# Performance work log

Hardware: AMD Instinct MI355X
Metric: run time of the kernel (lower is better)

Reference implementation:

```python
import jax, jax.numpy as jnp
import numpy as np

NEG_BIG = -9e15

def setup_inputs() -> dict:
    key = jax.random.key(0)
    kx, ka, kW, k1, k2 = jax.random.split(key, 5)
    B, N, F, H, D = 8, 1024, 1024, 16, 64
    x = jax.random.normal(kx, (B, N, F), dtype=jnp.float32)
    adj = jax.random.randint(ka, (B, N, N), 0, 2, dtype=jnp.int32)
    # xavier_uniform with gain=1.414
    gain = 1.414
    limW = gain * np.sqrt(6.0 / (F + D))
    lima = gain * np.sqrt(6.0 / (D + 1))
    W = jax.random.uniform(kW, (H, F, D), minval=-limW, maxval=limW, dtype=jnp.float32)
    a1 = jax.random.uniform(k1, (H, D), minval=-lima, maxval=lima, dtype=jnp.float32)
    a2 = jax.random.uniform(k2, (H, D), minval=-lima, maxval=lima, dtype=jnp.float32)
    return {"x": x, "adj": adj, "W": W, "a1": a1, "a2": a2}

def reference(x, adj, W, a1, a2):
    alpha = 0.2
    # Wh: [B, H, N, D]
    Wh = jnp.einsum('bnf,hfd->bhnd', x, W)
    f1 = jnp.einsum('bhnd,hd->bhn', Wh, a1)  # [B,H,N]
    f2 = jnp.einsum('bhnd,hd->bhn', Wh, a2)  # [B,H,N]
    e = f1[:, :, :, None] + f2[:, :, None, :]          # [B,H,N,N]
    e = jnp.where(e > 0, e, alpha * e)                  # leaky relu
    mask = (adj > 0)[:, None, :, :]                     # [B,1,N,N]
    scores = jnp.where(mask, e, NEG_BIG)
    attn = jax.nn.softmax(scores, axis=-1)              # [B,H,N,N]
    # dropout omitted (inference / training=False)
    h_prime = jnp.einsum('bhnm,bhmd->bhnd', attn, Wh)   # [B,H,N,D]
    B, H, N, D = h_prime.shape
    # concat heads along feature dim (matches torch.cat over dim=2)
    y = jnp.transpose(h_prime, (0, 2, 1, 3)).reshape(B, N, H * D)
    return y
```

## Files before the change

kernel.cpp:

```cpp
#include <hip/hip_runtime.h>

typedef float    f32x4 __attribute__((ext_vector_type(4)));
typedef short    s16x8 __attribute__((ext_vector_type(8)));
typedef _Float16 f16x8 __attribute__((ext_vector_type(8)));
typedef _Float16 f16x4 __attribute__((ext_vector_type(4)));
typedef unsigned int   u32x4 __attribute__((ext_vector_type(4)));


__device__ __forceinline__ unsigned short bf16rne(float f){
  unsigned u = __float_as_uint(f);
  return (unsigned short)((u + 0x7FFFu + ((u >> 16) & 1u)) >> 16);
}

__global__ __launch_bounds__(256) void prep_kernel(const int* __restrict__ adj,
    const float* __restrict__ x, const float* __restrict__ W,
    unsigned* __restrict__ maskb, unsigned short* __restrict__ xb,
    unsigned short* __restrict__ Wt)
{
  const int bid = blockIdx.x, tid = threadIdx.x;
  if (bid < 1024) {
    const int lane = tid & 63;
    int gw = (bid * 256 + tid) >> 6;
    for (int s = gw; s < 131072; s += 4096) {
      int a = adj[(size_t)s * 64 + lane];
      unsigned long long m = __ballot(a > 0);
      if (lane == 0) {
        maskb[s * 2]     = (unsigned)m;
        maskb[s * 2 + 1] = (unsigned)(m >> 32);
      }
    }
  } else if (bid < 5120) {
    int idx = ((bid - 1024) * 256 + tid) * 8;
    f32x4 v0 = *reinterpret_cast<const f32x4*>(&x[idx]);
    f32x4 v1 = *reinterpret_cast<const f32x4*>(&x[idx + 4]);
    u32x4 o;
    o[0] = (unsigned)bf16rne(v0[0]) | ((unsigned)bf16rne(v0[1]) << 16);
    o[1] = (unsigned)bf16rne(v0[2]) | ((unsigned)bf16rne(v0[3]) << 16);
    o[2] = (unsigned)bf16rne(v1[0]) | ((unsigned)bf16rne(v1[1]) << 16);
    o[3] = (unsigned)bf16rne(v1[2]) | ((unsigned)bf16rne(v1[3]) << 16);
    *reinterpret_cast<u32x4*>(&xb[idx]) = o;
  } else {
    __shared__ float t[16][17];
    int rel = bid - 5120;
    int f0 = (rel & 63) * 16, d0 = ((rel >> 6) & 3) * 16, hh = rel >> 8;
    const int tx = tid & 15, ty = tid >> 4;
    t[ty][tx] = W[(size_t)hh * 65536 + (size_t)(f0 + ty) * 64 + (d0 + tx)];
    __syncthreads();
    float v = t[tx][ty];
    size_t o = (size_t)(hh * 64 + d0 + ty) * 1024 + (f0 + tx);
    Wt[o] = bf16rne(v);
  }
}

#define GSTAGE(BUF, K0) { \
  _Pragma("unroll") \
  for (int r = 0; r < 2; ++r) { \
    int flat = r * 256 + tid; int row = flat >> 2; int o8 = (flat & 3) << 3; \
    *reinterpret_cast<u32x4*>(&Ah[BUF][row * 40 + o8]) = \
        *reinterpret_cast<const u32x4*>(&xb[(size_t)(m0 + row) * 1024 + (K0) + o8]); \
  } \
  _Pragma("unroll") \
  for (int r = 0; r < 2; ++r) { \
    int flat = r * 256 + tid; int row = flat >> 2; int o8 = (flat & 3) << 3; \
    *reinterpret_cast<u32x4*>(&Bh[BUF][row * 40 + o8]) = \
        *reinterpret_cast<const u32x4*>(&Btg[(size_t)(n0 + row) * 1024 + (K0) + o8]); \
  } }

__global__ __launch_bounds__(256, 3) void gemm_kernel(const unsigned short* __restrict__ xb,
    const unsigned short* __restrict__ Btg,
    const float* __restrict__ a1, const float* __restrict__ a2,
    _Float16* __restrict__ WhT, float* __restrict__ f1, float* __restrict__ f2)
{
  __shared__ unsigned short Ah[2][128 * 40], Bh[2][128 * 40];
  const int tid  = threadIdx.x;
  const int lane = tid & 63, wave = tid >> 6;
  const int m0 = blockIdx.x * 128, n0 = blockIdx.y * 128;
  const int wm = (wave & 1) * 64, wn = (wave >> 1) * 64;
  const int rA = lane & 15, kg = lane >> 4;

  f32x4 acc[4][4] = {};

  GSTAGE(0, 0);
  __syncthreads();
  int cur = 0;
  for (int k0 = 0; k0 < 1024; k0 += 32) {
    if (k0 + 32 < 1024) { GSTAGE(cur ^ 1, k0 + 32); }

    s16x8 ah[4], bh[4];
#pragma unroll
    for (int i = 0; i < 4; ++i)
      ah[i] = *reinterpret_cast<const s16x8*>(&Ah[cur][(wm + i * 16 + rA) * 40 + kg * 8]);
#pragma unroll
    for (int j = 0; j < 4; ++j)
      bh[j] = *reinterpret_cast<const s16x8*>(&Bh[cur][(wn + j * 16 + rA) * 40 + kg * 8]);
#pragma unroll
    for (int i = 0; i < 4; ++i)
#pragma unroll
      for (int j = 0; j < 4; ++j)
        acc[i][j] = __builtin_amdgcn_mfma_f32_16x16x32_bf16(ah[i], bh[j], acc[i][j], 0, 0, 0);
    __syncthreads();
    cur ^= 1;
  }

#pragma unroll
  for (int i = 0; i < 4; ++i) {
    int gm0 = m0 + wm + i * 16 + kg * 4;
#pragma unroll
    for (int j = 0; j < 4; ++j) {
      int gn = n0 + wn + j * 16 + rA;
      int bb = gm0 >> 10, nn = gm0 & 1023;
      int hh = gn >> 6,  dd = gn & 63;
      f16x4 hv;
#pragma unroll
      for (int jj = 0; jj < 4; ++jj) hv[jj] = (_Float16)acc[i][j][jj];
      *reinterpret_cast<f16x4*>(&WhT[((size_t)((bb * 16 + hh) * 64 + dd) << 10) + nn]) = hv;
    }
  }

  const int hw = (n0 + wn) >> 6;
  float a1v[4], a2v[4];
#pragma unroll
  for (int j = 0; j < 4; ++j) {
    int d = j * 16 + rA;
    a1v[j] = a1[hw * 64 + d];
    a2v[j] = a2[hw * 64 + d];
  }
#pragma unroll
  for (int i = 0; i < 4; ++i) {
#pragma unroll
    for (int jj = 0; jj < 4; ++jj) {
      float s1 = 0.f, s2 = 0.f;
#pragma unroll
      for (int j = 0; j < 4; ++j) {
        float v = acc[i][j][jj];
        s1 += v * a1v[j];
        s2 += v * a2v[j];
      }
#pragma unroll
      for (int off = 1; off < 16; off <<= 1) {
        s1 += __shfl_xor(s1, off);
        s2 += __shfl_xor(s2, off);
      }
      if (rA == 0) {
        int gm = m0 + wm + i * 16 + kg * 4 + jj;
        int bb = gm >> 10, nn = gm & 1023;
        size_t o = (size_t)(bb * 16 + hw) * 1024 + nn;
        f1[o] = s1;
        f2[o] = s2;
      }
    }
  }
}

#define PSTAGE(BUF, M0) { \
  _Pragma("unroll") \
  for (int r = 0; r < 2; ++r) { \
    int flat = r * 256 + tid; int d = flat >> 3; int o = (flat & 7) << 3; \
    *reinterpret_cast<u32x4*>(&Bsh[BUF][d * 72 + o]) = \
        *reinterpret_cast<const u32x4*>(&whtb[(size_t)d * 1024 + (M0) + o]); \
  } }

__global__ __launch_bounds__(256, 4) void pv_kernel(const _Float16* __restrict__ WhT,
    const float* __restrict__ f1, const float* __restrict__ f2,
    const unsigned* __restrict__ maskb, float* __restrict__ y)
{
  const int tid = threadIdx.x, lane = tid & 63, wave = tid >> 6;
  const int rb = blockIdx.x, h = blockIdx.y, b = blockIdx.z;
  const int bh = b * 16 + h;
  const int n0 = rb * 128;
  const _Float16* whtb = WhT + ((size_t)bh << 16);

  __shared__ _Float16 Bsh[2][64 * 72];
  __shared__ float Cs[1024], Ds[1024];
  __shared__ float smx[4];
  __shared__ unsigned long long lutm[16];

  const float K = 1.44269504f;

  float pmax;
  {
    f32x4 fv = *reinterpret_cast<const f32x4*>(&f2[(size_t)bh * 1024 + tid * 4]);
    f32x4 sv, cv, dv;
#pragma unroll
    for (int e = 0; e < 4; ++e) {
      sv[e] = fv[e] * K;
      cv[e] = __builtin_amdgcn_exp2f(sv[e]);
      dv[e] = __builtin_amdgcn_exp2f(0.2f * sv[e]);
    }
    *reinterpret_cast<f32x4*>(&Cs[tid * 4]) = cv;
    *reinterpret_cast<f32x4*>(&Ds[tid * 4]) = dv;
    pmax = fmaxf(fmaxf(sv[0], sv[1]), fmaxf(sv[2], sv[3]));
  }
#pragma unroll
  for (int off = 32; off; off >>= 1) pmax = fmaxf(pmax, __shfl_xor(pmax, off));
  if (lane == 0) smx[wave] = pmax;
  if (tid < 16) {
    unsigned lo = ((tid & 1) ? 0xFFFFu : 0u) | ((tid & 2) ? 0xFFFF0000u : 0u);
    unsigned hi = ((tid & 4) ? 0xFFFFu : 0u) | ((tid & 8) ? 0xFFFF0000u : 0u);
    lutm[tid] = ((unsigned long long)hi << 32) | lo;
  }
  __syncthreads();

  const float m2s = fmaxf(fmaxf(smx[0], smx[1]), fmaxf(smx[2], smx[3]));

  const int rA = lane & 15, kg = lane >> 4;
  const int wrow = wave * 32;
  f32x4 acc[2][4] = {};
  f32x4 dacc[2] = {};
  int   rloc[2];
  float At[2], Bt[2];
  const unsigned* mrow[2];
#pragma unroll
  for (int t = 0; t < 2; ++t) {
    rloc[t] = wrow + t * 16 + rA;
    float f1p = f1[(size_t)bh * 1024 + n0 + rloc[t]] * K;
    float sf = f1p + m2s;
    float Mp = fmaxf(sf, 0.2f * sf);
    At[t] = __builtin_amdgcn_exp2f(f1p - Mp);
    Bt[t] = __builtin_amdgcn_exp2f(0.2f * f1p - Mp);
    mrow[t] = maskb + ((size_t)(b << 10) + n0 + rloc[t]) * 32;
  }
  f16x8 ones;
#pragma unroll
  for (int e = 0; e < 8; ++e) ones[e] = (_Float16)1.0f;

  uint2 mwcur[2], mwnext[2];
#pragma unroll
  for (int t = 0; t < 2; ++t)
    mwcur[t] = *reinterpret_cast<const uint2*>(&mrow[t][0]);
  PSTAGE(0, 0);
  __syncthreads();
  int cur = 0;

  for (int m0 = 0; m0 < 1024; m0 += 64) {
    if (m0 + 64 < 1024) {
      PSTAGE(cur ^ 1, m0 + 64);
#pragma unroll
      for (int t = 0; t < 2; ++t)
        mwnext[t] = *reinterpret_cast<const uint2*>(&mrow[t][(m0 + 64) >> 5]);
    }
#pragma unroll
    for (int ks = 0; ks < 2; ++ks) {
      const int kc = m0 + ks * 32 + kg * 8;
      f32x4 ca = *reinterpret_cast<const f32x4*>(&Cs[kc]);
      f32x4 cb = *reinterpret_cast<const f32x4*>(&Cs[kc + 4]);
      f32x4 da = *reinterpret_cast<const f32x4*>(&Ds[kc]);
      f32x4 db = *reinterpret_cast<const f32x4*>(&Ds[kc + 4]);
      f16x8 pa[2];
#pragma unroll
      for (int t = 0; t < 2; ++t) {
        unsigned mw = (&mwcur[t].x)[ks] >> (kg * 8);
        f16x8 pt;
#pragma unroll
        for (int jj = 0; jj < 8; ++jj) {
          float C = (jj < 4) ? ca[jj] : cb[jj - 4];
          float D = (jj < 4) ? da[jj] : db[jj - 4];
          pt[jj] = (_Float16)fmaxf(At[t] * C, Bt[t] * D);
        }
        u32x4 pw = __builtin_bit_cast(u32x4, pt);
        unsigned long long mq0 = lutm[mw & 15u];
        unsigned long long mq1 = lutm[(mw >> 4) & 15u];
        pw[0] &= (unsigned)mq0;  pw[1] &= (unsigned)(mq0 >> 32);
        pw[2] &= (unsigned)mq1;  pw[3] &= (unsigned)(mq1 >> 32);
        pa[t] = __builtin_bit_cast(f16x8, pw);
        dacc[t] = __builtin_amdgcn_mfma_f32_16x16x32_f16(pa[t], ones, dacc[t], 0, 0, 0);
      }
#pragma unroll
      for (int j = 0; j < 4; ++j) {
        f16x8 bf = *reinterpret_cast<const f16x8*>(&Bsh[cur][(j * 16 + rA) * 72 + ks * 32 + kg * 8]);
        acc[0][j] = __builtin_amdgcn_mfma_f32_16x16x32_f16(pa[0], bf, acc[0][j], 0, 0, 0);
        acc[1][j] = __builtin_amdgcn_mfma_f32_16x16x32_f16(pa[1], bf, acc[1][j], 0, 0, 0);
      }
    }
    __syncthreads();
    cur ^= 1;
#pragma unroll
    for (int t = 0; t < 2; ++t) mwcur[t] = mwnext[t];
  }

#pragma unroll
  for (int t = 0; t < 2; ++t) {
    f32x4 rd;
#pragma unroll
    for (int jj = 0; jj < 4; ++jj) rd[jj] = dacc[t][jj] > 0.f ? 1.0f / dacc[t][jj] : 0.f;
#pragma unroll
    for (int j = 0; j < 4; ++j) {
#pragma unroll
      for (int jj = 0; jj < 4; ++jj) {
        int row = wrow + t * 16 + kg * 4 + jj;
        int n = n0 + row, d = j * 16 + rA;
        y[(((size_t)b * 1024 + n) << 10) + h * 64 + d] = acc[t][j][jj] * rd[jj];
      }
    }
  }
}

extern "C" void kernel_launch(void* const* d_in, const int* in_sizes, int n_in,
                              void* d_out, int out_size, void* d_ws, size_t ws_size,
                              hipStream_t stream)
{
  const float* x  = (const float*)d_in[0];
  const int*   adj = (const int*)d_in[1];
  const float* W  = (const float*)d_in[2];
  const float* a1 = (const float*)d_in[3];
  const float* a2 = (const float*)d_in[4];
  float* y = (float*)d_out;

  char* ws = (char*)d_ws;
  unsigned short* Wt = (unsigned short*)(ws);
  unsigned*       maskb = (unsigned*)(ws + ((size_t)2 << 20));
  float* f1   = (float*)(ws + ((size_t)3 << 20));
  float* f2   = (float*)(ws + ((size_t)3 << 20) + ((size_t)512 << 10));
  _Float16* WhT = (_Float16*)(ws + ((size_t)4 << 20));
  unsigned short* xb = (unsigned short*)(ws + ((size_t)20 << 20));

  prep_kernel<<<9216, 256, 0, stream>>>(adj, x, W, maskb, xb, Wt);
  gemm_kernel<<<dim3(64, 8), 256, 0, stream>>>(xb, Wt, a1, a2, WhT, f1, f2);
  pv_kernel<<<dim3(8, 16, 8), 256, 0, stream>>>(WhT, f1, f2, maskb, y);
}
```

Baseline: 93.23 us.

## Halve GEMM N-tile to 64, raise occupancy, and use packed f16 conversion in PV

The projection GEMM tile shrinks from 128x128 to 128x64 with four waves each owning 32 rows. This doubles the grid and cuts per-thread accumulators so the kernel can raise its launch bound to four blocks per CU. The aim is more resident waves and more blocks to fill the CUs, at the cost of more reloads of the A tile. In the PV kernel the C/D loads are hoisted ahead of both k-steps, and the f16 conversion now uses packed round-toward-zero cvt_pkrtz. That conversion cuts instruction count but changes rounding from round-to-nearest.

```diff
diff --git a/kernel.cpp b/kernel.cpp
--- a/kernel.cpp
+++ b/kernel.cpp
@@ -4,6 +4,7 @@
 typedef short    s16x8 __attribute__((ext_vector_type(8)));
 typedef _Float16 f16x8 __attribute__((ext_vector_type(8)));
 typedef _Float16 f16x4 __attribute__((ext_vector_type(4)));
+typedef _Float16 f16x2 __attribute__((ext_vector_type(2)));
 typedef unsigned int   u32x4 __attribute__((ext_vector_type(4)));
 
 
@@ -59,26 +60,24 @@
     *reinterpret_cast<u32x4*>(&Ah[BUF][row * 40 + o8]) = \
         *reinterpret_cast<const u32x4*>(&xb[(size_t)(m0 + row) * 1024 + (K0) + o8]); \
   } \
-  _Pragma("unroll") \
-  for (int r = 0; r < 2; ++r) { \
-    int flat = r * 256 + tid; int row = flat >> 2; int o8 = (flat & 3) << 3; \
+  { int row = tid >> 2; int o8 = (tid & 3) << 3; \
     *reinterpret_cast<u32x4*>(&Bh[BUF][row * 40 + o8]) = \
         *reinterpret_cast<const u32x4*>(&Btg[(size_t)(n0 + row) * 1024 + (K0) + o8]); \
   } }
 
-__global__ __launch_bounds__(256, 3) void gemm_kernel(const unsigned short* __restrict__ xb,
+__global__ __launch_bounds__(256, 4) void gemm_kernel(const unsigned short* __restrict__ xb,
     const unsigned short* __restrict__ Btg,
     const float* __restrict__ a1, const float* __restrict__ a2,
     _Float16* __restrict__ WhT, float* __restrict__ f1, float* __restrict__ f2)
 {
-  __shared__ unsigned short Ah[2][128 * 40], Bh[2][128 * 40];
+  __shared__ unsigned short Ah[2][128 * 40], Bh[2][64 * 40];
   const int tid  = threadIdx.x;
   const int lane = tid & 63, wave = tid >> 6;
-  const int m0 = blockIdx.x * 128, n0 = blockIdx.y * 128;
-  const int wm = (wave & 1) * 64, wn = (wave >> 1) * 64;
+  const int m0 = blockIdx.x * 128, n0 = blockIdx.y * 64;
+  const int wm = wave * 32;
   const int rA = lane & 15, kg = lane >> 4;
 
-  f32x4 acc[4][4] = {};
+  f32x4 acc[2][4] = {};
 
   GSTAGE(0, 0);
   __syncthreads();
@@ -86,15 +85,15 @@
   for (int k0 = 0; k0 < 1024; k0 += 32) {
     if (k0 + 32 < 1024) { GSTAGE(cur ^ 1, k0 + 32); }
 
-    s16x8 ah[4], bh[4];
-#pragma unroll
-    for (int i = 0; i < 4; ++i)
+    s16x8 ah[2], bh[4];
+#pragma unroll
+    for (int i = 0; i < 2; ++i)
       ah[i] = *reinterpret_cast<const s16x8*>(&Ah[cur][(wm + i * 16 + rA) * 40 + kg * 8]);
 #pragma unroll
     for (int j = 0; j < 4; ++j)
-      bh[j] = *reinterpret_cast<const s16x8*>(&Bh[cur][(wn + j * 16 + rA) * 40 + kg * 8]);
-#pragma unroll
-    for (int i = 0; i < 4; ++i)
+      bh[j] = *reinterpret_cast<const s16x8*>(&Bh[cur][(j * 16 + rA) * 40 + kg * 8]);
+#pragma unroll
+    for (int i = 0; i < 2; ++i)
 #pragma unroll
       for (int j = 0; j < 4; ++j)
         acc[i][j] = __builtin_amdgcn_mfma_f32_16x16x32_bf16(ah[i], bh[j], acc[i][j], 0, 0, 0);
@@ -103,11 +102,11 @@
   }
 
 #pragma unroll
-  for (int i = 0; i < 4; ++i) {
+  for (int i = 0; i < 2; ++i) {
     int gm0 = m0 + wm + i * 16 + kg * 4;
 #pragma unroll
     for (int j = 0; j < 4; ++j) {
-      int gn = n0 + wn + j * 16 + rA;
+      int gn = n0 + j * 16 + rA;
       int bb = gm0 >> 10, nn = gm0 & 1023;
       int hh = gn >> 6,  dd = gn & 63;
       f16x4 hv;
@@ -117,7 +116,7 @@
     }
   }
 
-  const int hw = (n0 + wn) >> 6;
+  const int hw = n0 >> 6;
   float a1v[4], a2v[4];
 #pragma unroll
   for (int j = 0; j < 4; ++j) {
@@ -126,7 +125,7 @@
     a2v[j] = a2[hw * 64 + d];
   }
 #pragma unroll
-  for (int i = 0; i < 4; ++i) {
+  for (int i = 0; i < 2; ++i) {
 #pragma unroll
     for (int jj = 0; jj < 4; ++jj) {
       float s1 = 0.f, s2 = 0.f;
@@ -239,25 +238,33 @@
       for (int t = 0; t < 2; ++t)
         mwnext[t] = *reinterpret_cast<const uint2*>(&mrow[t][(m0 + 64) >> 5]);
     }
+    f32x4 cd[2][4];
 #pragma unroll
     for (int ks = 0; ks < 2; ++ks) {
       const int kc = m0 + ks * 32 + kg * 8;
-      f32x4 ca = *reinterpret_cast<const f32x4*>(&Cs[kc]);
-      f32x4 cb = *reinterpret_cast<const f32x4*>(&Cs[kc + 4]);
-      f32x4 da = *reinterpret_cast<const f32x4*>(&Ds[kc]);
-      f32x4 db = *reinterpret_cast<const f32x4*>(&Ds[kc + 4]);
+      cd[ks][0] = *reinterpret_cast<const f32x4*>(&Cs[kc]);
+      cd[ks][1] = *reinterpret_cast<const f32x4*>(&Cs[kc + 4]);
+      cd[ks][2] = *reinterpret_cast<const f32x4*>(&Ds[kc]);
+      cd[ks][3] = *reinterpret_cast<const f32x4*>(&Ds[kc + 4]);
+    }
+#pragma unroll
+    for (int ks = 0; ks < 2; ++ks) {
       f16x8 pa[2];
 #pragma unroll
       for (int t = 0; t < 2; ++t) {
         unsigned mw = (&mwcur[t].x)[ks] >> (kg * 8);
-        f16x8 pt;
+        float pv_[8];
 #pragma unroll
         for (int jj = 0; jj < 8; ++jj) {
-          float C = (jj < 4) ? ca[jj] : cb[jj - 4];
-          float D = (jj < 4) ? da[jj] : db[jj - 4];
-          pt[jj] = (_Float16)fmaxf(At[t] * C, Bt[t] * D);
+          float C = (jj < 4) ? cd[ks][0][jj] : cd[ks][1][jj - 4];
+          float D = (jj < 4) ? cd[ks][2][jj] : cd[ks][3][jj - 4];
+          pv_[jj] = fmaxf(At[t] * C, Bt[t] * D);
         }
-        u32x4 pw = __builtin_bit_cast(u32x4, pt);
+        u32x4 pw;
+        pw[0] = __builtin_bit_cast(unsigned, __builtin_amdgcn_cvt_pkrtz(pv_[0], pv_[1]));
+        pw[1] = __builtin_bit_cast(unsigned, __builtin_amdgcn_cvt_pkrtz(pv_[2], pv_[3]));
+        pw[2] = __builtin_bit_cast(unsigned, __builtin_amdgcn_cvt_pkrtz(pv_[4], pv_[5]));
+        pw[3] = __builtin_bit_cast(unsigned, __builtin_amdgcn_cvt_pkrtz(pv_[6], pv_[7]));
         unsigned long long mq0 = lutm[mw & 15u];
         unsigned long long mq1 = lutm[(mw >> 4) & 15u];
         pw[0] &= (unsigned)mq0;  pw[1] &= (unsigned)(mq0 >> 32);
@@ -315,6 +322,6 @@
   unsigned short* xb = (unsigned short*)(ws + ((size_t)20 << 20));
 
   prep_kernel<<<9216, 256, 0, stream>>>(adj, x, W, maskb, xb, Wt);
-  gemm_kernel<<<dim3(64, 8), 256, 0, stream>>>(xb, Wt, a1, a2, WhT, f1, f2);
+  gemm_kernel<<<dim3(64, 16), 256, 0, stream>>>(xb, Wt, a1, a2, WhT, f1, f2);
   pv_kernel<<<dim3(8, 16, 8), 256, 0, stream>>>(WhT, f1, f2, maskb, y);
 }
```

Result: slower. 95.47 us (+2.4%).
